# Kernel tuning notes

Measured on AMD Instinct MI355X. Metric: run time of the kernel, lower is better.

Reference implementation:

```python
import jax, jax.numpy as jnp
import numpy as np

LN_EPS = 1e-5  # torch nn.LayerNorm default
ATT_EPS = 1e-8  # episilon added to sqrt(dk)

B, S, D = 16, 2048, 1024


def setup_inputs() -> dict:
    key = jax.random.key(0)
    ks = jax.random.split(key, 5)
    Q = jax.random.normal(ks[0], (B, S, D), dtype=jnp.float32)
    K = jax.random.normal(ks[1], (B, S, D), dtype=jnp.float32)
    V = jax.random.normal(ks[2], (B, S, D), dtype=jnp.float32)
    # xavier_normal for square DxD: std = sqrt(2/(D+D)) = 1/sqrt(D)
    std = 1.0 / np.sqrt(D)
    W1 = jax.random.normal(ks[3], (D, D), dtype=jnp.float32) * std
    W2 = jax.random.normal(ks[4], (D, D), dtype=jnp.float32) * std
    b1 = jnp.zeros((D,), dtype=jnp.float32)
    b2 = jnp.zeros((D,), dtype=jnp.float32)
    ln_gamma = jnp.ones((D,), dtype=jnp.float32)
    ln_beta = jnp.zeros((D,), dtype=jnp.float32)
    return {"Q": Q, "K": K, "V": V, "W1": W1, "b1": b1, "W2": W2, "b2": b2,
            "ln_gamma": ln_gamma, "ln_beta": ln_beta}


def _layer_norm(x, gamma, beta):
    mu = jnp.mean(x, axis=-1, keepdims=True)
    var = jnp.mean(jnp.square(x - mu), axis=-1, keepdims=True)
    return (x - mu) * jax.lax.rsqrt(var + LN_EPS) * gamma + beta


def reference(Q, K, V, W1, b1, W2, b2, ln_gamma, ln_beta):
    d = Q.shape[-1]
    scale = 1.0 / (jnp.sqrt(jnp.float32(max(1.0, d))) + ATT_EPS)
    # scores: (B, Sq, Sk)
    scores = jnp.einsum('bqd,bkd->bqk', Q, K) * scale
    attn = jax.nn.softmax(scores, axis=-1)
    V_att = jnp.einsum('bqk,bkd->bqd', attn, V)
    X = _layer_norm(Q + V_att, ln_gamma, ln_beta)
    ffn = jnp.einsum('bqd,ed->bqe', jax.nn.relu(jnp.einsum('bqd,hd->bqh', X, W1) + b1), W2) + b2
    return _layer_norm(ffn + X, ln_gamma, ln_beta)
```

## Files before the change

### kernel.cpp

```cpp
#include <hip/hip_runtime.h>
#include <cmath>
#include <cstdint>

#define LN_EPS 1e-5f

typedef __bf16 bf16x8 __attribute__((ext_vector_type(8)));
typedef float f32x4 __attribute__((ext_vector_type(4)));
typedef unsigned short u16x8 __attribute__((ext_vector_type(8)));
typedef unsigned short u16x4 __attribute__((ext_vector_type(4)));

__device__ inline float b2f(unsigned short u) {
    union { unsigned int ui; float f; } x; x.ui = ((unsigned int)u) << 16; return x.f;
}
__device__ inline unsigned short f2b(float f) {
    union { float f; unsigned int ui; } x; x.f = f;
    unsigned int u = x.ui;
    return (unsigned short)((u + 0x7FFFu + ((u >> 16) & 1u)) >> 16);
}

__global__ void cvt_kernel(const float* __restrict__ in, unsigned short* __restrict__ out,
                           long n, float scale) {
    long i = ((long)blockIdx.x * blockDim.x + threadIdx.x) * 8;
    long stride = (long)gridDim.x * blockDim.x * 8;
    for (; i < n; i += stride) {
        float4 a = *reinterpret_cast<const float4*>(in + i);
        float4 b = *reinterpret_cast<const float4*>(in + i + 4);
        u16x8 o;
        o[0] = f2b(a.x * scale); o[1] = f2b(a.y * scale); o[2] = f2b(a.z * scale); o[3] = f2b(a.w * scale);
        o[4] = f2b(b.x * scale); o[5] = f2b(b.y * scale); o[6] = f2b(b.z * scale); o[7] = f2b(b.w * scale);
        *reinterpret_cast<u16x8*>(out + i) = o;
    }
}

__global__ void transpose_kernel(const float* __restrict__ V, unsigned short* __restrict__ Vt,
                                 int S, int D) {
    __shared__ float t[32][33];
    int b = blockIdx.z;
    int s0 = blockIdx.x * 32, d0 = blockIdx.y * 32;
    int tx = threadIdx.x & 31, ty = threadIdx.x >> 5;
    const float* Vb = V + (long)b * S * D;
    unsigned short* Vtb = Vt + (long)b * S * D;
#pragma unroll
    for (int r = 0; r < 4; ++r)
        t[ty + r * 8][tx] = Vb[(long)(s0 + ty + r * 8) * D + d0 + tx];
    __syncthreads();
#pragma unroll
    for (int r = 0; r < 4; ++r)
        Vtb[(long)(d0 + ty + r * 8) * S + s0 + tx] = f2b(t[tx][ty + r * 8]);
}

#define GBK 64

__device__ inline void gload16(const unsigned short* g, unsigned short* l) {
    __builtin_amdgcn_global_load_lds((const __attribute__((address_space(1))) void*)g,
                                     (__attribute__((address_space(3))) void*)l, 16, 0, 0);
}

__device__ inline void stage_half(const unsigned short* gRowBase, int ldk, int k0,
                                  unsigned short* ldsHalf, int tid) {
#pragma unroll
    for (int l = 0; l < 2; ++l) {
        int g = l * 512 + tid;
        int row = g >> 3;
        int lg = (g & 7) ^ (row & 7);
        gload16(gRowBase + (long)row * ldk + k0 + lg * 8, ldsHalf + g * 8);
    }
}

__device__ inline bf16x8 frag_ld(const unsigned short* ldsHalf, int rowInHalf, int kgran) {
    int sw = kgran ^ (rowInHalf & 7);
    return *reinterpret_cast<const bf16x8*>(ldsHalf + rowInHalf * 64 + sw * 8);
}

#define GMFMA(am, bn, mi, ni) \
    acc[mi][ni] = __builtin_amdgcn_mfma_f32_16x16x32_bf16(am, bn, acc[mi][ni], 0, 0, 0)

template <int MODE>
__global__ __launch_bounds__(512, 1) void gemm256(
    const unsigned short* __restrict__ A, const unsigned short* __restrict__ B,
    void* __restrict__ Cout, const float* __restrict__ aux1, const float* __restrict__ aux2,
    float* __restrict__ aux3, float* __restrict__ aux4,
    int tX, int tY, int N, int K, long bsA, long bsB, long bsC, float scale) {
    extern __shared__ __align__(16) unsigned short lds[];
    const int cpx = gridDim.x >> 3;
    const int swz = (blockIdx.x & 7) * cpx + (blockIdx.x >> 3);
    const int bx = swz % tX;
    const int t2 = swz / tX;
    const int by = t2 % tY;
    const int bz = t2 / tY;

    const unsigned short* Ab = A + (long)bz * bsA + (long)by * 256 * K;
    const unsigned short* Bb = B + (long)bz * bsB + (long)bx * 256 * K;
    const int tid = threadIdx.x;
    const int wid = tid >> 6, lane = tid & 63;
    const int wr = wid >> 2, wc = wid & 3;
    const int lr = lane & 15, kq = lane >> 4;
    const int NT = K >> 6;
    const int ccol = lane & 15, crow0 = kq * 4;
    const long m0 = (long)by * 256 + wr * 128;
    const long n0 = (long)bx * 256 + wc * 64;

#define STAGE_A(tile, half) stage_half(Ab + (long)(half) * 128 * K, K, (tile) * GBK, \
        lds + (((tile) & 1) * 32768 + (half) * 8192), tid)
#define STAGE_B(tile, half) stage_half(Bb + (long)(half) * 128 * K, K, (tile) * GBK, \
        lds + (((tile) & 1) * 32768 + 16384 + (half) * 8192), tid)

    f32x4 acc[8][4];
#pragma unroll
    for (int i = 0; i < 8; ++i)
#pragma unroll
        for (int j = 0; j < 4; ++j) acc[i][j] = (f32x4){0.f, 0.f, 0.f, 0.f};
    bf16x8 a[4][2], b[4][2];

    STAGE_A(0, 0); STAGE_A(0, 1); STAGE_B(0, 0); STAGE_B(0, 1);
    STAGE_B(1, 0); STAGE_A(1, 0);
    asm volatile("s_waitcnt vmcnt(4)" ::: "memory");
    __builtin_amdgcn_s_barrier();

    for (int t = 0; t < NT; ++t) {
        const unsigned short* aB = lds + ((t & 1) * 32768 + wr * 8192);
        const unsigned short* bB = lds + ((t & 1) * 32768 + 16384 + (wc >> 1) * 8192);
        const int bRow0 = (wc & 1) * 64;
#pragma unroll
        for (int m = 0; m < 4; ++m)
#pragma unroll
            for (int ks = 0; ks < 2; ++ks)
                a[m][ks] = frag_ld(aB, m * 16 + lr, ks * 4 + kq);
#pragma unroll
        for (int n = 0; n < 2; ++n)
#pragma unroll
            for (int ks = 0; ks < 2; ++ks)
                b[n][ks] = frag_ld(bB, bRow0 + n * 16 + lr, ks * 4 + kq);
        if (t + 1 < NT) STAGE_A(t + 1, 1);
        __builtin_amdgcn_s_barrier();
        asm volatile("s_waitcnt lgkmcnt(0)" ::: "memory");
        __builtin_amdgcn_sched_barrier(0);
        __builtin_amdgcn_s_setprio(1);
#pragma unroll
        for (int m = 0; m < 4; ++m)
#pragma unroll
            for (int n = 0; n < 2; ++n)
#pragma unroll
                for (int ks = 0; ks < 2; ++ks) GMFMA(a[m][ks], b[n][ks], m, n);
        __builtin_amdgcn_s_setprio(0);
        __builtin_amdgcn_s_barrier();
#pragma unroll
        for (int n = 0; n < 2; ++n)
#pragma unroll
            for (int ks = 0; ks < 2; ++ks)
                b[2 + n][ks] = frag_ld(bB, bRow0 + (2 + n) * 16 + lr, ks * 4 + kq);
        if (t + 1 < NT) STAGE_B(t + 1, 1);
        __builtin_amdgcn_s_barrier();
        asm volatile("s_waitcnt lgkmcnt(0)" ::: "memory");
        __builtin_amdgcn_sched_barrier(0);
        __builtin_amdgcn_s_setprio(1);
#pragma unroll
        for (int m = 0; m < 4; ++m)
#pragma unroll
            for (int n = 0; n < 2; ++n)
#pragma unroll
                for (int ks = 0; ks < 2; ++ks) GMFMA(a[m][ks], b[2 + n][ks], m, 2 + n);
        __builtin_amdgcn_s_setprio(0);
        __builtin_amdgcn_s_barrier();
#pragma unroll
        for (int m = 0; m < 4; ++m)
#pragma unroll
            for (int ks = 0; ks < 2; ++ks)
                a[m][ks] = frag_ld(aB, 64 + m * 16 + lr, ks * 4 + kq);
        if (t + 2 < NT) STAGE_B(t + 2, 0);
        __builtin_amdgcn_s_barrier();
        asm volatile("s_waitcnt lgkmcnt(0)" ::: "memory");
        __builtin_amdgcn_sched_barrier(0);
        __builtin_amdgcn_s_setprio(1);
#pragma unroll
        for (int m = 0; m < 4; ++m)
#pragma unroll
            for (int n = 0; n < 2; ++n)
#pragma unroll
                for (int ks = 0; ks < 2; ++ks) GMFMA(a[m][ks], b[n][ks], 4 + m, n);
        __builtin_amdgcn_s_setprio(0);
        __builtin_amdgcn_s_barrier();
        if (t + 2 < NT) STAGE_A(t + 2, 0);
        if (t < NT - 2) asm volatile("s_waitcnt vmcnt(4)" ::: "memory");
        else            asm volatile("s_waitcnt vmcnt(0)" ::: "memory");
        __builtin_amdgcn_s_barrier();
        __builtin_amdgcn_s_setprio(1);
#pragma unroll
        for (int m = 0; m < 4; ++m)
#pragma unroll
            for (int n = 0; n < 2; ++n)
#pragma unroll
                for (int ks = 0; ks < 2; ++ks) GMFMA(a[m][ks], b[2 + n][ks], 4 + m, 2 + n);
        __builtin_amdgcn_s_setprio(0);
        __builtin_amdgcn_s_barrier();
    }

    if (MODE == 0) {
        float* sl = (float*)lds;
        unsigned short* Pout = (unsigned short*)Cout;
#pragma unroll
        for (int m = 0; m < 8; ++m) {
            float ls[4] = {0.f, 0.f, 0.f, 0.f};
#pragma unroll
            for (int n = 0; n < 4; ++n) {
                long gn = n0 + n * 16 + ccol;
#pragma unroll
                for (int r = 0; r < 4; ++r) {
                    float p = __expf(acc[m][n][r]);
                    ls[r] += p;
                    Pout[bz * bsC + (m0 + m * 16 + crow0 + r) * N + gn] = f2b(p);
                }
            }
#pragma unroll
            for (int r = 0; r < 4; ++r)
#pragma unroll
                for (int off = 8; off >= 1; off >>= 1) ls[r] += __shfl_xor(ls[r], off, 64);
            if ((lane & 15) == 0)
#pragma unroll
                for (int r = 0; r < 4; ++r)
                    sl[wc * 256 + wr * 128 + m * 16 + crow0 + r] = ls[r];
        }
        __syncthreads();
        if (wc == 0) {
#pragma unroll
            for (int rep = 0; rep < 2; ++rep) {
                int rowB = wr * 128 + rep * 64 + lane;
                float s4 = sl[0 * 256 + rowB] + sl[1 * 256 + rowB] +
                           sl[2 * 256 + rowB] + sl[3 * 256 + rowB];
                ((float*)aux1)[((long)bz * 8 + bx) * 2048 + by * 256 + rowB] = s4;
            }
        }
        return;
    }

    if (MODE == 1) {
        const float* il = aux2 + (long)bz * 2048 + m0;
        float* sls = (float*)lds;
        float* slq = sls + 1024;
        unsigned short* Xout = (unsigned short*)Cout;
#pragma unroll
        for (int m = 0; m < 8; ++m) {
            float ls[4] = {0.f, 0.f, 0.f, 0.f}, lq[4] = {0.f, 0.f, 0.f, 0.f};
#pragma unroll
            for (int r = 0; r < 4; ++r) {
                float cf = il[m * 16 + crow0 + r];
                long gm = m0 + m * 16 + crow0 + r;
#pragma unroll
                for (int n = 0; n < 4; ++n) {
                    long gn = n0 + n * 16 + ccol;
                    long idx = bz * bsC + gm * N + gn;
                    float v = acc[m][n][r] * cf +
                              b2f(((const unsigned short*)aux1)[idx]) * scale;
                    Xout[idx] = f2b(v);
                    ls[r] += v; lq[r] += v * v;
                }
            }
#pragma unroll
            for (int r = 0; r < 4; ++r)
#pragma unroll
                for (int off = 8; off >= 1; off >>= 1) {
                    ls[r] += __shfl_xor(ls[r], off, 64);
                    lq[r] += __shfl_xor(lq[r], off, 64);
                }
            if ((lane & 15) == 0)
#pragma unroll
                for (int r = 0; r < 4; ++r) {
                    sls[wc * 256 + wr * 128 + m * 16 + crow0 + r] = ls[r];
                    slq[wc * 256 + wr * 128 + m * 16 + crow0 + r] = lq[r];
                }
        }
        __syncthreads();
        if (wc == 0) {
#pragma unroll
            for (int rep = 0; rep < 2; ++rep) {
                int rowB = wr * 128 + rep * 64 + lane;
                float s4 = sls[rowB] + sls[256 + rowB] + sls[512 + rowB] + sls[768 + rowB];
                float q4 = slq[rowB] + slq[256 + rowB] + slq[512 + rowB] + slq[768 + rowB];
                long sidx = ((long)bz * 4 + bx) * 2048 + by * 256 + rowB;
                aux3[sidx] = s4;
                aux4[sidx] = q4;
            }
        }
        return;
    }

#pragma unroll
    for (int m = 0; m < 8; ++m) {
#pragma unroll
        for (int n = 0; n < 4; ++n) {
            long gn = n0 + n * 16 + ccol;
#pragma unroll
            for (int r = 0; r < 4; ++r) {
                long gm = m0 + m * 16 + crow0 + r;
                float v = acc[m][n][r];
                if (MODE == 2) {
                    ((unsigned short*)Cout)[gm * N + gn] = f2b(fmaxf(v + aux1[gn], 0.f));
                } else {
                    long idx = gm * N + gn;
                    ((unsigned short*)Cout)[idx] =
                        f2b(v + aux1[gn] + b2f(((const unsigned short*)aux2)[idx]));
                }
            }
        }
    }
#undef STAGE_A
#undef STAGE_B
}

__global__ void suminv_kernel(const float* __restrict__ stats, float* __restrict__ invL) {
    int i = blockIdx.x * 256 + threadIdx.x;
    int bz = i >> 11, row = i & 2047;
    long base = (long)bz * 8 * 2048 + row;
    float L = 0.f;
#pragma unroll
    for (int t = 0; t < 8; ++t) L += stats[base + t * 2048];
    invL[i] = 1.f / L;
}

__global__ void lnstats_kernel(const float* __restrict__ ss, const float* __restrict__ sq,
                               float* __restrict__ mu, float* __restrict__ rs) {
    int i = blockIdx.x * 256 + threadIdx.x;
    int bz = i >> 11, row = i & 2047;
    long base = (long)bz * 4 * 2048 + row;
    float s = 0.f, q = 0.f;
#pragma unroll
    for (int t = 0; t < 4; ++t) { s += ss[base + t * 2048]; q += sq[base + t * 2048]; }
    float m = s * (1.f / 1024.f);
    float var = q * (1.f / 1024.f) - m * m;
    mu[i] = m;
    rs[i] = rsqrtf(var + LN_EPS);
}

__global__ void ln_apply_kernel(unsigned short* __restrict__ X, const float* __restrict__ mu,
                                const float* __restrict__ rs, const float* __restrict__ gamma,
                                const float* __restrict__ beta) {
    long i = ((long)blockIdx.x * 256 + threadIdx.x) * 8;
    int row = (int)(i >> 10), col = (int)(i & 1023);
    float m = mu[row], r = rs[row];
    u16x8 raw = *reinterpret_cast<const u16x8*>(X + i);
    float4 g0 = *reinterpret_cast<const float4*>(gamma + col);
    float4 g1 = *reinterpret_cast<const float4*>(gamma + col + 4);
    float4 b0 = *reinterpret_cast<const float4*>(beta + col);
    float4 b1 = *reinterpret_cast<const float4*>(beta + col + 4);
    u16x8 o;
    o[0] = f2b((b2f(raw[0]) - m) * r * g0.x + b0.x);
    o[1] = f2b((b2f(raw[1]) - m) * r * g0.y + b0.y);
    o[2] = f2b((b2f(raw[2]) - m) * r * g0.z + b0.z);
    o[3] = f2b((b2f(raw[3]) - m) * r * g0.w + b0.w);
    o[4] = f2b((b2f(raw[4]) - m) * r * g1.x + b1.x);
    o[5] = f2b((b2f(raw[5]) - m) * r * g1.y + b1.y);
    o[6] = f2b((b2f(raw[6]) - m) * r * g1.z + b1.z);
    o[7] = f2b((b2f(raw[7]) - m) * r * g1.w + b1.w);
    *reinterpret_cast<u16x8*>(X + i) = o;
}

__device__ inline float wave_sum(float v) {
#pragma unroll
    for (int off = 32; off > 0; off >>= 1) v += __shfl_xor(v, off, 64);
    return v;
}

__global__ void ln_final_kernel(const unsigned short* __restrict__ Yb,
                                const float* __restrict__ gamma, const float* __restrict__ beta,
                                float* __restrict__ out) {
    __shared__ float red[8];
    long row = blockIdx.x;
    const unsigned short* y = Yb + row * 1024;
    int tid = threadIdx.x;
    int wv = tid >> 6, ln = tid & 63;
    u16x4 raw = *reinterpret_cast<const u16x4*>(y + tid * 4);
    float v0 = b2f(raw[0]), v1 = b2f(raw[1]), v2 = b2f(raw[2]), v3 = b2f(raw[3]);
    float s = v0 + v1 + v2 + v3;
    float q = v0 * v0 + v1 * v1 + v2 * v2 + v3 * v3;
    s = wave_sum(s);
    q = wave_sum(q);
    if (ln == 0) { red[wv] = s; red[4 + wv] = q; }
    __syncthreads();
    s = red[0] + red[1] + red[2] + red[3];
    q = red[4] + red[5] + red[6] + red[7];
    float mu = s * (1.f / 1024.f);
    float var = q * (1.f / 1024.f) - mu * mu;
    float rsg = rsqrtf(var + LN_EPS);
    float4 g = *reinterpret_cast<const float4*>(gamma + tid * 4);
    float4 b = *reinterpret_cast<const float4*>(beta + tid * 4);
    float4 o;
    o.x = (v0 - mu) * rsg * g.x + b.x;
    o.y = (v1 - mu) * rsg * g.y + b.y;
    o.z = (v2 - mu) * rsg * g.z + b.z;
    o.w = (v3 - mu) * rsg * g.w + b.w;
    *reinterpret_cast<float4*>(out + row * 1024 + tid * 4) = o;
}

extern "C" void kernel_launch(void* const* d_in, const int* in_sizes, int n_in,
                              void* d_out, int out_size, void* d_ws, size_t ws_size,
                              hipStream_t stream) {
    const float* Q     = (const float*)d_in[0];
    const float* K     = (const float*)d_in[1];
    const float* V     = (const float*)d_in[2];
    const float* W1    = (const float*)d_in[3];
    const float* b1    = (const float*)d_in[4];
    const float* W2    = (const float*)d_in[5];
    const float* b2    = (const float*)d_in[6];
    const float* gamma = (const float*)d_in[7];
    const float* beta  = (const float*)d_in[8];
    float* out = (float*)d_out;

    const int Bq = 16, S = 2048, D = 1024;
    const long SD = (long)S * D;
    const long SS = (long)S * S;
    const long rows = (long)Bq * S;

    const size_t NEED = 3 * (size_t)(Bq * SD * 2) + 2 * (size_t)D * D * 2 + (size_t)(Bq * SS * 2);
    if (ws_size < NEED) return;

    char* ws = (char*)d_ws;
    unsigned short* Qb  = (unsigned short*)ws; ws += Bq * SD * 2;
    unsigned short* Kb  = (unsigned short*)ws; ws += Bq * SD * 2;
    unsigned short* Vt  = (unsigned short*)ws; ws += Bq * SD * 2;
    unsigned short* W1b = (unsigned short*)ws; ws += (long)D * D * 2;
    unsigned short* W2b = (unsigned short*)ws; ws += (long)D * D * 2;
    unsigned short* Sb  = (unsigned short*)ws; ws += Bq * SS * 2;

    unsigned short* Xb = Qb;
    unsigned short* H  = Kb;
    unsigned short* Yb = (unsigned short*)Sb;

    char* sc = (char*)W1b;
    float* stats   = (float*)sc;
    float* invL    = (float*)(sc + 0x100000);
    float* stats_s = (float*)(sc + 0x140000);
    float* stats_q = (float*)(sc + 0x1C0000);
    float* muArr   = (float*)(sc + 0x240000);
    float* rsArr   = (float*)(sc + 0x260000);

    const int DYN_LDS = 131072;
    (void)hipFuncSetAttribute(reinterpret_cast<const void*>(&gemm256<0>),
                              hipFuncAttributeMaxDynamicSharedMemorySize, DYN_LDS);
    (void)hipFuncSetAttribute(reinterpret_cast<const void*>(&gemm256<1>),
                              hipFuncAttributeMaxDynamicSharedMemorySize, DYN_LDS);
    (void)hipFuncSetAttribute(reinterpret_cast<const void*>(&gemm256<2>),
                              hipFuncAttributeMaxDynamicSharedMemorySize, DYN_LDS);
    (void)hipFuncSetAttribute(reinterpret_cast<const void*>(&gemm256<3>),
                              hipFuncAttributeMaxDynamicSharedMemorySize, DYN_LDS);

    const float scale = 1.0f / (sqrtf((float)D) + 1e-8f);
    const float rescale = sqrtf((float)D) + 1e-8f;

    cvt_kernel<<<1024, 256, 0, stream>>>(Q, Qb, Bq * SD, scale);
    cvt_kernel<<<1024, 256, 0, stream>>>(K, Kb, Bq * SD, 1.0f);
    transpose_kernel<<<dim3(S / 32, D / 32, Bq), 256, 0, stream>>>(V, Vt, S, D);

    gemm256<0><<<1024, 512, DYN_LDS, stream>>>(
        Qb, Kb, Sb, stats, nullptr, nullptr, nullptr, 8, 8, S, D, SD, SD, SS, 1.0f);
    suminv_kernel<<<128, 256, 0, stream>>>(stats, invL);

    gemm256<1><<<512, 512, DYN_LDS, stream>>>(
        Sb, Vt, Xb, (const float*)Qb, invL, stats_s, stats_q, 4, 8, D, S, SS, SD, SD, rescale);
    lnstats_kernel<<<128, 256, 0, stream>>>(stats_s, stats_q, muArr, rsArr);
    ln_apply_kernel<<<16384, 256, 0, stream>>>(Xb, muArr, rsArr, gamma, beta);

    cvt_kernel<<<512, 256, 0, stream>>>(W1, W1b, (long)D * D, 1.0f);
    cvt_kernel<<<512, 256, 0, stream>>>(W2, W2b, (long)D * D, 1.0f);

    gemm256<2><<<512, 512, DYN_LDS, stream>>>(
        Xb, W1b, H, b1, nullptr, nullptr, nullptr, 4, 128, D, D, 0, 0, 0, 1.0f);
    gemm256<3><<<512, 512, DYN_LDS, stream>>>(
        H, W2b, Yb, b2, (const float*)Xb, nullptr, nullptr, 4, 128, D, D, 0, 0, 0, 1.0f);
    ln_final_kernel<<<rows, 256, 0, stream>>>(Yb, gamma, beta, out);
}
```

Baseline: 629.4 us.

## Make GEMM persistent over multiple N tiles and fold small stat kernels into consumers

Each GEMM workgroup now walks several consecutive output tiles along N and reuses the same A rows. The K-loop prefetch runs on into the next tile's B so the pipeline never drains between tiles, and grids shrink to 256 workgroups. The separate 1/L reduction moves into the PV GEMM prologue, LayerNorm stats move into ln_apply, and paired fp32-to-bf16 conversions merge into one launch. This cuts launch count and pipeline prologue/epilogue cost, but the epilogue now runs inside the main loop, which raises register pressure and code size, and 256 workgroups may underfill the device's CUs.

```diff
diff --git a/kernel.cpp b/kernel.cpp
--- a/kernel.cpp
+++ b/kernel.cpp
@@ -18,17 +18,23 @@
     return (unsigned short)((u + 0x7FFFu + ((u >> 16) & 1u)) >> 16);
 }
 
-__global__ void cvt_kernel(const float* __restrict__ in, unsigned short* __restrict__ out,
-                           long n, float scale) {
+__global__ void cvt2_kernel(const float* __restrict__ ia, unsigned short* __restrict__ oa,
+                            long na, float sa,
+                            const float* __restrict__ ib, unsigned short* __restrict__ ob,
+                            long nb) {
     long i = ((long)blockIdx.x * blockDim.x + threadIdx.x) * 8;
     long stride = (long)gridDim.x * blockDim.x * 8;
+    long n = na + nb;
     for (; i < n; i += stride) {
-        float4 a = *reinterpret_cast<const float4*>(in + i);
-        float4 b = *reinterpret_cast<const float4*>(in + i + 4);
+        const float* in; unsigned short* out; long j; float s;
+        if (i < na) { in = ia; out = oa; j = i; s = sa; }
+        else        { in = ib; out = ob; j = i - na; s = 1.0f; }
+        float4 a = *reinterpret_cast<const float4*>(in + j);
+        float4 b = *reinterpret_cast<const float4*>(in + j + 4);
         u16x8 o;
-        o[0] = f2b(a.x * scale); o[1] = f2b(a.y * scale); o[2] = f2b(a.z * scale); o[3] = f2b(a.w * scale);
-        o[4] = f2b(b.x * scale); o[5] = f2b(b.y * scale); o[6] = f2b(b.z * scale); o[7] = f2b(b.w * scale);
-        *reinterpret_cast<u16x8*>(out + i) = o;
+        o[0] = f2b(a.x * s); o[1] = f2b(a.y * s); o[2] = f2b(a.z * s); o[3] = f2b(a.w * s);
+        o[4] = f2b(b.x * s); o[5] = f2b(b.y * s); o[6] = f2b(b.z * s); o[7] = f2b(b.w * s);
+        *reinterpret_cast<u16x8*>(out + j) = o;
     }
 }
 
@@ -80,30 +86,33 @@
     const unsigned short* __restrict__ A, const unsigned short* __restrict__ B,
     void* __restrict__ Cout, const float* __restrict__ aux1, const float* __restrict__ aux2,
     float* __restrict__ aux3, float* __restrict__ aux4,
-    int tX, int tY, int N, int K, long bsA, long bsB, long bsC, float scale) {
+    int tX, int tY, int N, int K, long bsA, long bsB, long bsC, float scale, int TPB) {
     extern __shared__ __align__(16) unsigned short lds[];
     const int cpx = gridDim.x >> 3;
     const int swz = (blockIdx.x & 7) * cpx + (blockIdx.x >> 3);
-    const int bx = swz % tX;
-    const int t2 = swz / tX;
-    const int by = t2 % tY;
-    const int bz = t2 / tY;
+    const int t0 = swz * TPB;
+    const int bx0 = t0 % tX;
+    const int byz = t0 / tX;
+    const int by = byz % tY, bz = byz / tY;
 
     const unsigned short* Ab = A + (long)bz * bsA + (long)by * 256 * K;
-    const unsigned short* Bb = B + (long)bz * bsB + (long)bx * 256 * K;
+    const unsigned short* BbC = B + (long)bz * bsB + (long)bx0 * 256 * K;
+    const unsigned short* BbN = BbC + (TPB > 1 ? (long)256 * K : 0);
+
     const int tid = threadIdx.x;
     const int wid = tid >> 6, lane = tid & 63;
     const int wr = wid >> 2, wc = wid & 3;
     const int lr = lane & 15, kq = lane >> 4;
     const int NT = K >> 6;
+    const int TOT = TPB * NT;
     const int ccol = lane & 15, crow0 = kq * 4;
     const long m0 = (long)by * 256 + wr * 128;
-    const long n0 = (long)bx * 256 + wc * 64;
-
-#define STAGE_A(tile, half) stage_half(Ab + (long)(half) * 128 * K, K, (tile) * GBK, \
-        lds + (((tile) & 1) * 32768 + (half) * 8192), tid)
-#define STAGE_B(tile, half) stage_half(Bb + (long)(half) * 128 * K, K, (tile) * GBK, \
-        lds + (((tile) & 1) * 32768 + 16384 + (half) * 8192), tid)
+    const int bRow0 = (wc & 1) * 64;
+
+#define SA0(kt, dst) stage_half(Ab, K, (kt) * GBK, dst, tid)
+#define SA1(kt, dst) stage_half(Ab + (long)128 * K, K, (kt) * GBK, dst, tid)
+#define SB0(base, kt, dst) stage_half(base, K, (kt) * GBK, dst, tid)
+#define SB1(base, kt, dst) stage_half(base + (long)128 * K, K, (kt) * GBK, dst, tid)
 
     f32x4 acc[8][4];
 #pragma unroll
@@ -112,15 +121,37 @@
         for (int j = 0; j < 4; ++j) acc[i][j] = (f32x4){0.f, 0.f, 0.f, 0.f};
     bf16x8 a[4][2], b[4][2];
 
-    STAGE_A(0, 0); STAGE_A(0, 1); STAGE_B(0, 0); STAGE_B(0, 1);
-    STAGE_B(1, 0); STAGE_A(1, 0);
-    asm volatile("s_waitcnt vmcnt(4)" ::: "memory");
+    if (MODE == 1) {
+        float* invLl = (float*)(lds + 69632);
+        if (tid < 256) {
+            int row = by * 256 + tid;
+            float L = 0.f;
+#pragma unroll
+            for (int x = 0; x < 8; ++x) L += aux2[((long)bz * 8 + x) * 2048 + row];
+            invLl[tid] = 1.f / L;
+        }
+    }
+
+    SA0(0, lds);            SA1(0, lds + 8192);
+    SB0(BbC, 0, lds + 16384); SB1(BbC, 0, lds + 24576);
+    SB0(BbC, 1, lds + 32768 + 16384);
+    SA0(1, lds + 32768);
+    asm volatile("s_waitcnt vmcnt(4) lgkmcnt(0)" ::: "memory");
     __builtin_amdgcn_s_barrier();
 
-    for (int t = 0; t < NT; ++t) {
-        const unsigned short* aB = lds + ((t & 1) * 32768 + wr * 8192);
-        const unsigned short* bB = lds + ((t & 1) * 32768 + 16384 + (wc >> 1) * 8192);
-        const int bRow0 = (wc & 1) * 64;
+    int k = 0, ti = 0;
+    for (int ft = 0; ft < TOT; ++ft) {
+        const unsigned short* aB = lds + ((ft & 1) * 32768 + wr * 8192);
+        const unsigned short* bB = lds + ((ft & 1) * 32768 + 16384 + (wc >> 1) * 8192);
+        unsigned short* buf1 = lds + ((ft + 1) & 1) * 32768;
+        unsigned short* buf2 = lds + (ft & 1) * 32768;
+        const bool s1 = (ft + 1 < TOT), s2 = (ft + 2 < TOT);
+        const bool in1 = (k + 1 < NT), in2 = (k + 2 < NT);
+        const int k1 = in1 ? k + 1 : 0;
+        const int k2 = in2 ? k + 2 : k + 2 - NT;
+        const unsigned short* B1 = in1 ? BbC : BbN;
+        const unsigned short* B2 = in2 ? BbC : BbN;
+
 #pragma unroll
         for (int m = 0; m < 4; ++m)
 #pragma unroll
@@ -131,7 +162,7 @@
 #pragma unroll
             for (int ks = 0; ks < 2; ++ks)
                 b[n][ks] = frag_ld(bB, bRow0 + n * 16 + lr, ks * 4 + kq);
-        if (t + 1 < NT) STAGE_A(t + 1, 1);
+        if (s1) SA1(k1, buf1 + 8192);
         __builtin_amdgcn_s_barrier();
         asm volatile("s_waitcnt lgkmcnt(0)" ::: "memory");
         __builtin_amdgcn_sched_barrier(0);
@@ -149,7 +180,7 @@
 #pragma unroll
             for (int ks = 0; ks < 2; ++ks)
                 b[2 + n][ks] = frag_ld(bB, bRow0 + (2 + n) * 16 + lr, ks * 4 + kq);
-        if (t + 1 < NT) STAGE_B(t + 1, 1);
+        if (s1) SB1(B1, k1, buf1 + 24576);
         __builtin_amdgcn_s_barrier();
         asm volatile("s_waitcnt lgkmcnt(0)" ::: "memory");
         __builtin_amdgcn_sched_barrier(0);
@@ -167,7 +198,7 @@
 #pragma unroll
             for (int ks = 0; ks < 2; ++ks)
                 a[m][ks] = frag_ld(aB, 64 + m * 16 + lr, ks * 4 + kq);
-        if (t + 2 < NT) STAGE_B(t + 2, 0);
+        if (s2) SB0(B2, k2, buf2 + 16384);
         __builtin_amdgcn_s_barrier();
         asm volatile("s_waitcnt lgkmcnt(0)" ::: "memory");
         __builtin_amdgcn_sched_barrier(0);
@@ -180,9 +211,9 @@
                 for (int ks = 0; ks < 2; ++ks) GMFMA(a[m][ks], b[n][ks], 4 + m, n);
         __builtin_amdgcn_s_setprio(0);
         __builtin_amdgcn_s_barrier();
-        if (t + 2 < NT) STAGE_A(t + 2, 0);
-        if (t < NT - 2) asm volatile("s_waitcnt vmcnt(4)" ::: "memory");
-        else            asm volatile("s_waitcnt vmcnt(0)" ::: "memory");
+        if (s2) SA0(k2, buf2);
+        if (ft < TOT - 2) asm volatile("s_waitcnt vmcnt(4)" ::: "memory");
+        else              asm volatile("s_waitcnt vmcnt(0)" ::: "memory");
         __builtin_amdgcn_s_barrier();
         __builtin_amdgcn_s_setprio(1);
 #pragma unroll
@@ -193,150 +224,156 @@
                 for (int ks = 0; ks < 2; ++ks) GMFMA(a[m][ks], b[2 + n][ks], 4 + m, 2 + n);
         __builtin_amdgcn_s_setprio(0);
         __builtin_amdgcn_s_barrier();
-    }
-
-    if (MODE == 0) {
-        float* sl = (float*)lds;
-        unsigned short* Pout = (unsigned short*)Cout;
-#pragma unroll
-        for (int m = 0; m < 8; ++m) {
-            float ls[4] = {0.f, 0.f, 0.f, 0.f};
-#pragma unroll
-            for (int n = 0; n < 4; ++n) {
-                long gn = n0 + n * 16 + ccol;
-#pragma unroll
-                for (int r = 0; r < 4; ++r) {
-                    float p = __expf(acc[m][n][r]);
-                    ls[r] += p;
-                    Pout[bz * bsC + (m0 + m * 16 + crow0 + r) * N + gn] = f2b(p);
+
+        if (k == NT - 1) {
+            const int bx = bx0 + ti;
+            const long n0 = (long)bx * 256 + wc * 64;
+            if (MODE == 0) {
+                float* sl = (float*)(lds + 65536);
+                unsigned short* Pout = (unsigned short*)Cout;
+#pragma unroll
+                for (int m = 0; m < 8; ++m) {
+                    float ls[4] = {0.f, 0.f, 0.f, 0.f};
+#pragma unroll
+                    for (int n = 0; n < 4; ++n) {
+                        long gn = n0 + n * 16 + ccol;
+#pragma unroll
+                        for (int r = 0; r < 4; ++r) {
+                            float p = __expf(acc[m][n][r]);
+                            ls[r] += p;
+                            Pout[bz * bsC + (m0 + m * 16 + crow0 + r) * N + gn] = f2b(p);
+                        }
+                    }
+#pragma unroll
+                    for (int r = 0; r < 4; ++r)
+#pragma unroll
+                        for (int off = 8; off >= 1; off >>= 1) ls[r] += __shfl_xor(ls[r], off, 64);
+                    if ((lane & 15) == 0)
+#pragma unroll
+                        for (int r = 0; r < 4; ++r)
+                            sl[wc * 256 + wr * 128 + m * 16 + crow0 + r] = ls[r];
+                }
+                __syncthreads();
+                if (wc == 0) {
+#pragma unroll
+                    for (int rep = 0; rep < 2; ++rep) {
+                        int rowB = wr * 128 + rep * 64 + lane;
+                        float s4 = sl[0 * 256 + rowB] + sl[1 * 256 + rowB] +
+                                   sl[2 * 256 + rowB] + sl[3 * 256 + rowB];
+                        ((float*)aux1)[((long)bz * tX + bx) * 2048 + by * 256 + rowB] = s4;
+                    }
+                }
+            } else if (MODE == 1) {
+                const float* invLl = (const float*)(lds + 69632);
+                float* sls = (float*)(lds + 65536);
+                float* slq = sls + 1024;
+                unsigned short* Xout = (unsigned short*)Cout;
+#pragma unroll
+                for (int m = 0; m < 8; ++m) {
+                    float ls[4] = {0.f, 0.f, 0.f, 0.f}, lq[4] = {0.f, 0.f, 0.f, 0.f};
+#pragma unroll
+                    for (int r = 0; r < 4; ++r) {
+                        float cf = invLl[wr * 128 + m * 16 + crow0 + r];
+                        long gm = m0 + m * 16 + crow0 + r;
+#pragma unroll
+                        for (int n = 0; n < 4; ++n) {
+                            long gn = n0 + n * 16 + ccol;
+                            long idx = bz * bsC + gm * N + gn;
+                            float v = acc[m][n][r] * cf +
+                                      b2f(((const unsigned short*)aux1)[idx]) * scale;
+                            Xout[idx] = f2b(v);
+                            ls[r] += v; lq[r] += v * v;
+                        }
+                    }
+#pragma unroll
+                    for (int r = 0; r < 4; ++r)
+#pragma unroll
+                        for (int off = 8; off >= 1; off >>= 1) {
+                            ls[r] += __shfl_xor(ls[r], off, 64);
+                            lq[r] += __shfl_xor(lq[r], off, 64);
+                        }
+                    if ((lane & 15) == 0)
+#pragma unroll
+                        for (int r = 0; r < 4; ++r) {
+                            sls[wc * 256 + wr * 128 + m * 16 + crow0 + r] = ls[r];
+                            slq[wc * 256 + wr * 128 + m * 16 + crow0 + r] = lq[r];
+                        }
+                }
+                __syncthreads();
+                if (wc == 0) {
+#pragma unroll
+                    for (int rep = 0; rep < 2; ++rep) {
+                        int rowB = wr * 128 + rep * 64 + lane;
+                        float s4 = sls[rowB] + sls[256 + rowB] + sls[512 + rowB] + sls[768 + rowB];
+                        float q4 = slq[rowB] + slq[256 + rowB] + slq[512 + rowB] + slq[768 + rowB];
+                        long sidx = ((long)bz * tX + bx) * 2048 + by * 256 + rowB;
+                        aux3[sidx] = s4;
+                        aux4[sidx] = q4;
+                    }
+                }
+            } else {
+#pragma unroll
+                for (int m = 0; m < 8; ++m) {
+#pragma unroll
+                    for (int n = 0; n < 4; ++n) {
+                        long gn = n0 + n * 16 + ccol;
+#pragma unroll
+                        for (int r = 0; r < 4; ++r) {
+                            long gm = m0 + m * 16 + crow0 + r;
+                            float v = acc[m][n][r];
+                            if (MODE == 2) {
+                                ((unsigned short*)Cout)[gm * N + gn] =
+                                    f2b(fmaxf(v + aux1[gn], 0.f));
+                            } else {
+                                long idx = gm * N + gn;
+                                ((unsigned short*)Cout)[idx] =
+                                    f2b(v + aux1[gn] + b2f(((const unsigned short*)aux2)[idx]));
+                            }
+                        }
+                    }
                 }
             }
 #pragma unroll
-            for (int r = 0; r < 4; ++r)
-#pragma unroll
-                for (int off = 8; off >= 1; off >>= 1) ls[r] += __shfl_xor(ls[r], off, 64);
-            if ((lane & 15) == 0)
-#pragma unroll
-                for (int r = 0; r < 4; ++r)
-                    sl[wc * 256 + wr * 128 + m * 16 + crow0 + r] = ls[r];
-        }
-        __syncthreads();
-        if (wc == 0) {
-#pragma unroll
-            for (int rep = 0; rep < 2; ++rep) {
-                int rowB = wr * 128 + rep * 64 + lane;
-                float s4 = sl[0 * 256 + rowB] + sl[1 * 256 + rowB] +
-                           sl[2 * 256 + rowB] + sl[3 * 256 + rowB];
-                ((float*)aux1)[((long)bz * 8 + bx) * 2048 + by * 256 + rowB] = s4;
-            }
-        }
-        return;
-    }
-
-    if (MODE == 1) {
-        const float* il = aux2 + (long)bz * 2048 + m0;
-        float* sls = (float*)lds;
-        float* slq = sls + 1024;
-        unsigned short* Xout = (unsigned short*)Cout;
-#pragma unroll
-        for (int m = 0; m < 8; ++m) {
-            float ls[4] = {0.f, 0.f, 0.f, 0.f}, lq[4] = {0.f, 0.f, 0.f, 0.f};
-#pragma unroll
-            for (int r = 0; r < 4; ++r) {
-                float cf = il[m * 16 + crow0 + r];
-                long gm = m0 + m * 16 + crow0 + r;
-#pragma unroll
-                for (int n = 0; n < 4; ++n) {
-                    long gn = n0 + n * 16 + ccol;
-                    long idx = bz * bsC + gm * N + gn;
-                    float v = acc[m][n][r] * cf +
-                              b2f(((const unsigned short*)aux1)[idx]) * scale;
-                    Xout[idx] = f2b(v);
-                    ls[r] += v; lq[r] += v * v;
-                }
-            }
-#pragma unroll
-            for (int r = 0; r < 4; ++r)
-#pragma unroll
-                for (int off = 8; off >= 1; off >>= 1) {
-                    ls[r] += __shfl_xor(ls[r], off, 64);
-                    lq[r] += __shfl_xor(lq[r], off, 64);
-                }
-            if ((lane & 15) == 0)
-#pragma unroll
-                for (int r = 0; r < 4; ++r) {
-                    sls[wc * 256 + wr * 128 + m * 16 + crow0 + r] = ls[r];
-                    slq[wc * 256 + wr * 128 + m * 16 + crow0 + r] = lq[r];
-                }
-        }
-        __syncthreads();
-        if (wc == 0) {
-#pragma unroll
-            for (int rep = 0; rep < 2; ++rep) {
-                int rowB = wr * 128 + rep * 64 + lane;
-                float s4 = sls[rowB] + sls[256 + rowB] + sls[512 + rowB] + sls[768 + rowB];
-                float q4 = slq[rowB] + slq[256 + rowB] + slq[512 + rowB] + slq[768 + rowB];
-                long sidx = ((long)bz * 4 + bx) * 2048 + by * 256 + rowB;
-                aux3[sidx] = s4;
-                aux4[sidx] = q4;
-            }
-        }
-        return;
-    }
-
-#pragma unroll
-    for (int m = 0; m < 8; ++m) {
-#pragma unroll
-        for (int n = 0; n < 4; ++n) {
-            long gn = n0 + n * 16 + ccol;
-#pragma unroll
-            for (int r = 0; r < 4; ++r) {
-                long gm = m0 + m * 16 + crow0 + r;
-                float v = acc[m][n][r];
-                if (MODE == 2) {
-                    ((unsigned short*)Cout)[gm * N + gn] = f2b(fmaxf(v + aux1[gn], 0.f));
-                } else {
-                    long idx = gm * N + gn;
-                    ((unsigned short*)Cout)[idx] =
-                        f2b(v + aux1[gn] + b2f(((const unsigned short*)aux2)[idx]));
-                }
-            }
+            for (int i = 0; i < 8; ++i)
+#pragma unroll
+                for (int j = 0; j < 4; ++j) acc[i][j] = (f32x4){0.f, 0.f, 0.f, 0.f};
+            ++ti;
+            BbC = BbN;
+            if (ti + 1 < TPB) BbN += (long)256 * K;
+            k = 0;
+        } else {
+            ++k;
         }
     }
-#undef STAGE_A
-#undef STAGE_B
-}
-
-__global__ void suminv_kernel(const float* __restrict__ stats, float* __restrict__ invL) {
-    int i = blockIdx.x * 256 + threadIdx.x;
-    int bz = i >> 11, row = i & 2047;
-    long base = (long)bz * 8 * 2048 + row;
-    float L = 0.f;
-#pragma unroll
-    for (int t = 0; t < 8; ++t) L += stats[base + t * 2048];
-    invL[i] = 1.f / L;
-}
-
-__global__ void lnstats_kernel(const float* __restrict__ ss, const float* __restrict__ sq,
-                               float* __restrict__ mu, float* __restrict__ rs) {
-    int i = blockIdx.x * 256 + threadIdx.x;
-    int bz = i >> 11, row = i & 2047;
-    long base = (long)bz * 4 * 2048 + row;
-    float s = 0.f, q = 0.f;
-#pragma unroll
-    for (int t = 0; t < 4; ++t) { s += ss[base + t * 2048]; q += sq[base + t * 2048]; }
-    float m = s * (1.f / 1024.f);
-    float var = q * (1.f / 1024.f) - m * m;
-    mu[i] = m;
-    rs[i] = rsqrtf(var + LN_EPS);
-}
-
-__global__ void ln_apply_kernel(unsigned short* __restrict__ X, const float* __restrict__ mu,
-                                const float* __restrict__ rs, const float* __restrict__ gamma,
+#undef SA0
+#undef SA1
+#undef SB0
+#undef SB1
+}
+
+__global__ void ln_apply_kernel(unsigned short* __restrict__ X, const float* __restrict__ ss,
+                                const float* __restrict__ sq, const float* __restrict__ gamma,
                                 const float* __restrict__ beta) {
-    long i = ((long)blockIdx.x * 256 + threadIdx.x) * 8;
-    int row = (int)(i >> 10), col = (int)(i & 1023);
-    float m = mu[row], r = rs[row];
+    __shared__ float mr[4];
+    int tid = threadIdx.x;
+    long rowbase = (long)blockIdx.x * 2;
+    if (tid < 2) {
+        long row = rowbase + tid;
+        int bz = (int)(row >> 11), lrow = (int)(row & 2047);
+        long base = (long)bz * 4 * 2048 + lrow;
+        float s = 0.f, q = 0.f;
+#pragma unroll
+        for (int t = 0; t < 4; ++t) { s += ss[base + t * 2048]; q += sq[base + t * 2048]; }
+        float m = s * (1.f / 1024.f);
+        float var = q * (1.f / 1024.f) - m * m;
+        mr[tid * 2] = m;
+        mr[tid * 2 + 1] = rsqrtf(var + LN_EPS);
+    }
+    __syncthreads();
+    int sub = tid >> 7;
+    float m = mr[sub * 2], r = mr[sub * 2 + 1];
+    long i = rowbase * 1024 + (long)tid * 8;
+    int col = (tid * 8) & 1023;
     u16x8 raw = *reinterpret_cast<const u16x8*>(X + i);
     float4 g0 = *reinterpret_cast<const float4*>(gamma + col);
     float4 g1 = *reinterpret_cast<const float4*>(gamma + col + 4);
@@ -395,7 +432,7 @@
                               void* d_out, int out_size, void* d_ws, size_t ws_size,
                               hipStream_t stream) {
     const float* Q     = (const float*)d_in[0];
-    const float* K     = (const float*)d_in[1];
+    const float* Kin   = (const float*)d_in[1];
     const float* V     = (const float*)d_in[2];
     const float* W1    = (const float*)d_in[3];
     const float* b1    = (const float*)d_in[4];
@@ -427,13 +464,10 @@
 
     char* sc = (char*)W1b;
     float* stats   = (float*)sc;
-    float* invL    = (float*)(sc + 0x100000);
     float* stats_s = (float*)(sc + 0x140000);
     float* stats_q = (float*)(sc + 0x1C0000);
-    float* muArr   = (float*)(sc + 0x240000);
-    float* rsArr   = (float*)(sc + 0x260000);
-
-    const int DYN_LDS = 131072;
+
+    const int DYN_LDS = 140288;
     (void)hipFuncSetAttribute(reinterpret_cast<const void*>(&gemm256<0>),
                               hipFuncAttributeMaxDynamicSharedMemorySize, DYN_LDS);
     (void)hipFuncSetAttribute(reinterpret_cast<const void*>(&gemm256<1>),
@@ -446,25 +480,22 @@
     const float scale = 1.0f / (sqrtf((float)D) + 1e-8f);
     const float rescale = sqrtf((float)D) + 1e-8f;
 
-    cvt_kernel<<<1024, 256, 0, stream>>>(Q, Qb, Bq * SD, scale);
-    cvt_kernel<<<1024, 256, 0, stream>>>(K, Kb, Bq * SD, 1.0f);
+    cvt2_kernel<<<2048, 256, 0, stream>>>(Q, Qb, Bq * SD, scale, Kin, Kb, Bq * SD);
     transpose_kernel<<<dim3(S / 32, D / 32, Bq), 256, 0, stream>>>(V, Vt, S, D);
 
-    gemm256<0><<<1024, 512, DYN_LDS, stream>>>(
-        Qb, Kb, Sb, stats, nullptr, nullptr, nullptr, 8, 8, S, D, SD, SD, SS, 1.0f);
-    suminv_kernel<<<128, 256, 0, stream>>>(stats, invL);
-
-    gemm256<1><<<512, 512, DYN_LDS, stream>>>(
-        Sb, Vt, Xb, (const float*)Qb, invL, stats_s, stats_q, 4, 8, D, S, SS, SD, SD, rescale);
-    lnstats_kernel<<<128, 256, 0, stream>>>(stats_s, stats_q, muArr, rsArr);
-    ln_apply_kernel<<<16384, 256, 0, stream>>>(Xb, muArr, rsArr, gamma, beta);
-
-    cvt_kernel<<<512, 256, 0, stream>>>(W1, W1b, (long)D * D, 1.0f);
-    cvt_kernel<<<512, 256, 0, stream>>>(W2, W2b, (long)D * D, 1.0f);
-
-    gemm256<2><<<512, 512, DYN_LDS, stream>>>(
-        Xb, W1b, H, b1, nullptr, nullptr, nullptr, 4, 128, D, D, 0, 0, 0, 1.0f);
-    gemm256<3><<<512, 512, DYN_LDS, stream>>>(
-        H, W2b, Yb, b2, (const float*)Xb, nullptr, nullptr, 4, 128, D, D, 0, 0, 0, 1.0f);
+    gemm256<0><<<256, 512, DYN_LDS, stream>>>(
+        Qb, Kb, Sb, stats, nullptr, nullptr, nullptr, 8, 8, S, D, SD, SD, SS, 1.0f, 4);
+
+    gemm256<1><<<256, 512, DYN_LDS, stream>>>(
+        Sb, Vt, Xb, (const float*)Qb, stats, stats_s, stats_q, 4, 8, D, S, SS, SD, SD,
+        rescale, 2);
+    ln_apply_kernel<<<16384, 256, 0, stream>>>(Xb, stats_s, stats_q, gamma, beta);
+
+    cvt2_kernel<<<512, 256, 0, stream>>>(W1, W1b, (long)D * D, 1.0f, W2, W2b, (long)D * D);
+
+    gemm256<2><<<256, 512, DYN_LDS, stream>>>(
+        Xb, W1b, H, b1, nullptr, nullptr, nullptr, 4, 128, D, D, 0, 0, 0, 1.0f, 2);
+    gemm256<3><<<256, 512, DYN_LDS, stream>>>(
+        H, W2b, Yb, b2, (const float*)Xb, nullptr, nullptr, 4, 128, D, D, 0, 0, 0, 1.0f, 2);
     ln_final_kernel<<<rows, 256, 0, stream>>>(Yb, gamma, beta, out);
 }
```

Measured after the change: 638.7 us. No clear change (+1.5%).

## Trim GEMM main-loop barriers, merge conversion launches, fold LN stats into apply

Applied to the files above, without the earlier changes.

The GEMM main loop drops several s_barrier and setprio transitions per K-tile. It issues the next-next A and B stage loads together, then merges the last two MFMA phases into one prioritized block with a single wait. Separately, the Q/K and W1/W2 bf16 conversions are merged into one launch each. The LayerNorm statistics reduction is folded into the apply kernel, removing a launch and a global intermediate. Fewer barriers should cut wave stalls, but earlier LDS staging into the buffer still being read may open a race between waves.

```diff
diff --git a/kernel.cpp b/kernel.cpp
--- a/kernel.cpp
+++ b/kernel.cpp
@@ -18,17 +18,23 @@
     return (unsigned short)((u + 0x7FFFu + ((u >> 16) & 1u)) >> 16);
 }
 
-__global__ void cvt_kernel(const float* __restrict__ in, unsigned short* __restrict__ out,
-                           long n, float scale) {
+__global__ void cvt2_kernel(const float* __restrict__ ia, unsigned short* __restrict__ oa,
+                            long na, float sa,
+                            const float* __restrict__ ib, unsigned short* __restrict__ ob,
+                            long nb) {
     long i = ((long)blockIdx.x * blockDim.x + threadIdx.x) * 8;
     long stride = (long)gridDim.x * blockDim.x * 8;
+    long n = na + nb;
     for (; i < n; i += stride) {
-        float4 a = *reinterpret_cast<const float4*>(in + i);
-        float4 b = *reinterpret_cast<const float4*>(in + i + 4);
+        const float* in; unsigned short* out; long j; float s;
+        if (i < na) { in = ia; out = oa; j = i; s = sa; }
+        else        { in = ib; out = ob; j = i - na; s = 1.0f; }
+        float4 a = *reinterpret_cast<const float4*>(in + j);
+        float4 b = *reinterpret_cast<const float4*>(in + j + 4);
         u16x8 o;
-        o[0] = f2b(a.x * scale); o[1] = f2b(a.y * scale); o[2] = f2b(a.z * scale); o[3] = f2b(a.w * scale);
-        o[4] = f2b(b.x * scale); o[5] = f2b(b.y * scale); o[6] = f2b(b.z * scale); o[7] = f2b(b.w * scale);
-        *reinterpret_cast<u16x8*>(out + i) = o;
+        o[0] = f2b(a.x * s); o[1] = f2b(a.y * s); o[2] = f2b(a.z * s); o[3] = f2b(a.w * s);
+        o[4] = f2b(b.x * s); o[5] = f2b(b.y * s); o[6] = f2b(b.z * s); o[7] = f2b(b.w * s);
+        *reinterpret_cast<u16x8*>(out + j) = o;
     }
 }
 
@@ -86,8 +92,7 @@
     const int swz = (blockIdx.x & 7) * cpx + (blockIdx.x >> 3);
     const int bx = swz % tX;
     const int t2 = swz / tX;
-    const int by = t2 % tY;
-    const int bz = t2 / tY;
+    const int by = t2 % tY, bz = t2 / tY;
 
     const unsigned short* Ab = A + (long)bz * bsA + (long)by * 256 * K;
     const unsigned short* Bb = B + (long)bz * bsB + (long)bx * 256 * K;
@@ -99,6 +104,7 @@
     const int ccol = lane & 15, crow0 = kq * 4;
     const long m0 = (long)by * 256 + wr * 128;
     const long n0 = (long)bx * 256 + wc * 64;
+    const int bRow0 = (wc & 1) * 64;
 
 #define STAGE_A(tile, half) stage_half(Ab + (long)(half) * 128 * K, K, (tile) * GBK, \
         lds + (((tile) & 1) * 32768 + (half) * 8192), tid)
@@ -120,7 +126,6 @@
     for (int t = 0; t < NT; ++t) {
         const unsigned short* aB = lds + ((t & 1) * 32768 + wr * 8192);
         const unsigned short* bB = lds + ((t & 1) * 32768 + 16384 + (wc >> 1) * 8192);
-        const int bRow0 = (wc & 1) * 64;
 #pragma unroll
         for (int m = 0; m < 4; ++m)
 #pragma unroll
@@ -143,7 +148,6 @@
 #pragma unroll
                 for (int ks = 0; ks < 2; ++ks) GMFMA(a[m][ks], b[n][ks], m, n);
         __builtin_amdgcn_s_setprio(0);
-        __builtin_amdgcn_s_barrier();
 #pragma unroll
         for (int n = 0; n < 2; ++n)
 #pragma unroll
@@ -161,13 +165,14 @@
 #pragma unroll
                 for (int ks = 0; ks < 2; ++ks) GMFMA(a[m][ks], b[2 + n][ks], m, 2 + n);
         __builtin_amdgcn_s_setprio(0);
-        __builtin_amdgcn_s_barrier();
 #pragma unroll
         for (int m = 0; m < 4; ++m)
 #pragma unroll
             for (int ks = 0; ks < 2; ++ks)
                 a[m][ks] = frag_ld(aB, 64 + m * 16 + lr, ks * 4 + kq);
-        if (t + 2 < NT) STAGE_B(t + 2, 0);
+        if (t + 2 < NT) { STAGE_B(t + 2, 0); STAGE_A(t + 2, 0); }
+        if (t < NT - 2) asm volatile("s_waitcnt vmcnt(4)" ::: "memory");
+        else            asm volatile("s_waitcnt vmcnt(0)" ::: "memory");
         __builtin_amdgcn_s_barrier();
         asm volatile("s_waitcnt lgkmcnt(0)" ::: "memory");
         __builtin_amdgcn_sched_barrier(0);
@@ -178,13 +183,6 @@
             for (int n = 0; n < 2; ++n)
 #pragma unroll
                 for (int ks = 0; ks < 2; ++ks) GMFMA(a[m][ks], b[n][ks], 4 + m, n);
-        __builtin_amdgcn_s_setprio(0);
-        __builtin_amdgcn_s_barrier();
-        if (t + 2 < NT) STAGE_A(t + 2, 0);
-        if (t < NT - 2) asm volatile("s_waitcnt vmcnt(4)" ::: "memory");
-        else            asm volatile("s_waitcnt vmcnt(0)" ::: "memory");
-        __builtin_amdgcn_s_barrier();
-        __builtin_amdgcn_s_setprio(1);
 #pragma unroll
         for (int m = 0; m < 4; ++m)
 #pragma unroll
@@ -192,7 +190,6 @@
 #pragma unroll
                 for (int ks = 0; ks < 2; ++ks) GMFMA(a[m][ks], b[2 + n][ks], 4 + m, 2 + n);
         __builtin_amdgcn_s_setprio(0);
-        __builtin_amdgcn_s_barrier();
     }
 
     if (MODE == 0) {
@@ -317,26 +314,29 @@
     invL[i] = 1.f / L;
 }
 
-__global__ void lnstats_kernel(const float* __restrict__ ss, const float* __restrict__ sq,
-                               float* __restrict__ mu, float* __restrict__ rs) {
-    int i = blockIdx.x * 256 + threadIdx.x;
-    int bz = i >> 11, row = i & 2047;
-    long base = (long)bz * 4 * 2048 + row;
-    float s = 0.f, q = 0.f;
-#pragma unroll
-    for (int t = 0; t < 4; ++t) { s += ss[base + t * 2048]; q += sq[base + t * 2048]; }
-    float m = s * (1.f / 1024.f);
-    float var = q * (1.f / 1024.f) - m * m;
-    mu[i] = m;
-    rs[i] = rsqrtf(var + LN_EPS);
-}
-
-__global__ void ln_apply_kernel(unsigned short* __restrict__ X, const float* __restrict__ mu,
-                                const float* __restrict__ rs, const float* __restrict__ gamma,
+__global__ void ln_apply_kernel(unsigned short* __restrict__ X, const float* __restrict__ ss,
+                                const float* __restrict__ sq, const float* __restrict__ gamma,
                                 const float* __restrict__ beta) {
-    long i = ((long)blockIdx.x * 256 + threadIdx.x) * 8;
-    int row = (int)(i >> 10), col = (int)(i & 1023);
-    float m = mu[row], r = rs[row];
+    __shared__ float mr[4];
+    int tid = threadIdx.x;
+    long rowbase = (long)blockIdx.x * 2;
+    if (tid < 2) {
+        long row = rowbase + tid;
+        int bz = (int)(row >> 11), lrow = (int)(row & 2047);
+        long base = (long)bz * 4 * 2048 + lrow;
+        float s = 0.f, q = 0.f;
+#pragma unroll
+        for (int t = 0; t < 4; ++t) { s += ss[base + t * 2048]; q += sq[base + t * 2048]; }
+        float m = s * (1.f / 1024.f);
+        float var = q * (1.f / 1024.f) - m * m;
+        mr[tid * 2] = m;
+        mr[tid * 2 + 1] = rsqrtf(var + LN_EPS);
+    }
+    __syncthreads();
+    int sub = tid >> 7;
+    float m = mr[sub * 2], r = mr[sub * 2 + 1];
+    long i = rowbase * 1024 + (long)tid * 8;
+    int col = (tid * 8) & 1023;
     u16x8 raw = *reinterpret_cast<const u16x8*>(X + i);
     float4 g0 = *reinterpret_cast<const float4*>(gamma + col);
     float4 g1 = *reinterpret_cast<const float4*>(gamma + col + 4);
@@ -395,7 +395,7 @@
                               void* d_out, int out_size, void* d_ws, size_t ws_size,
                               hipStream_t stream) {
     const float* Q     = (const float*)d_in[0];
-    const float* K     = (const float*)d_in[1];
+    const float* Kin   = (const float*)d_in[1];
     const float* V     = (const float*)d_in[2];
     const float* W1    = (const float*)d_in[3];
     const float* b1    = (const float*)d_in[4];
@@ -430,8 +430,6 @@
     float* invL    = (float*)(sc + 0x100000);
     float* stats_s = (float*)(sc + 0x140000);
     float* stats_q = (float*)(sc + 0x1C0000);
-    float* muArr   = (float*)(sc + 0x240000);
-    float* rsArr   = (float*)(sc + 0x260000);
 
     const int DYN_LDS = 131072;
     (void)hipFuncSetAttribute(reinterpret_cast<const void*>(&gemm256<0>),
@@ -446,8 +444,7 @@
     const float scale = 1.0f / (sqrtf((float)D) + 1e-8f);
     const float rescale = sqrtf((float)D) + 1e-8f;
 
-    cvt_kernel<<<1024, 256, 0, stream>>>(Q, Qb, Bq * SD, scale);
-    cvt_kernel<<<1024, 256, 0, stream>>>(K, Kb, Bq * SD, 1.0f);
+    cvt2_kernel<<<2048, 256, 0, stream>>>(Q, Qb, Bq * SD, scale, Kin, Kb, Bq * SD);
     transpose_kernel<<<dim3(S / 32, D / 32, Bq), 256, 0, stream>>>(V, Vt, S, D);
 
     gemm256<0><<<1024, 512, DYN_LDS, stream>>>(
@@ -456,11 +453,9 @@
 
     gemm256<1><<<512, 512, DYN_LDS, stream>>>(
         Sb, Vt, Xb, (const float*)Qb, invL, stats_s, stats_q, 4, 8, D, S, SS, SD, SD, rescale);
-    lnstats_kernel<<<128, 256, 0, stream>>>(stats_s, stats_q, muArr, rsArr);
-    ln_apply_kernel<<<16384, 256, 0, stream>>>(Xb, muArr, rsArr, gamma, beta);
-
-    cvt_kernel<<<512, 256, 0, stream>>>(W1, W1b, (long)D * D, 1.0f);
-    cvt_kernel<<<512, 256, 0, stream>>>(W2, W2b, (long)D * D, 1.0f);
+    ln_apply_kernel<<<16384, 256, 0, stream>>>(Xb, stats_s, stats_q, gamma, beta);
+
+    cvt2_kernel<<<512, 256, 0, stream>>>(W1, W1b, (long)D * D, 1.0f, W2, W2b, (long)D * D);
 
     gemm256<2><<<512, 512, DYN_LDS, stream>>>(
         Xb, W1b, H, b1, nullptr, nullptr, nullptr, 4, 128, D, D, 0, 0, 0, 1.0f);
```

New measurement: 631.0 us. Within noise of the previous version (+0.3%).
